# Kernel tuning notes

Measured on AMD Instinct MI355X. Metric: run time of the kernel, lower is better.

The kernel has to match this reference:

```python
import jax, jax.numpy as jnp
import numpy as np

H = 256
EPS = 1e-5
RBF_GAMMA = 10.0
RBF_CENTERS = jnp.asarray(np.arange(0.0, np.pi, 0.1), dtype=jnp.float32)  # 32 centers


def layer_norm(x, g, b):
    m = x.mean(-1, keepdims=True)
    v = ((x - m) ** 2).mean(-1, keepdims=True)
    return (x - m) * jax.lax.rsqrt(v + EPS) * g + b


def gin(src, dst, n_nodes, node_feat, edge_feat, w1, b1, w2, b2):
    # message = h_src + h_edge ; sum-aggregate at dst ; 2-layer MLP
    msg = node_feat[src] + edge_feat                                  # [E, H]
    agg = jax.ops.segment_sum(msg, dst, num_segments=n_nodes)        # [N, H]
    return jax.nn.relu(agg @ w1 + b1) @ w2 + b2


def graph_normal(gid, n_graphs, x):
    # divide each node feature by sqrt(#nodes in its graph)
    cnt = jax.ops.segment_sum(jnp.ones((x.shape[0],), x.dtype), gid, num_segments=n_graphs)
    return x * jax.lax.rsqrt(jnp.maximum(cnt, 1.0))[gid][:, None]


def geognn_block(src, dst, gid, n_graphs, node_hidden, edge_feat, w1, b1, w2, b2, ln_g, ln_b):
    out = gin(src, dst, node_hidden.shape[0], node_hidden, edge_feat, w1, b1, w2, b2)
    out = layer_norm(out, ln_g, ln_b)
    out = graph_normal(gid, n_graphs, out)
    # activation=False, dropout is identity in eval mode
    return out + node_hidden


def setup_inputs() -> dict:
    key = jax.random.key(0)
    ks = jax.random.split(key, 24)
    N, E, A, G = 65536, 131072, 262144, 2048
    nC = RBF_CENTERS.shape[0]
    s = 1.0 / np.sqrt(H)
    inp = {
        "node_hidden": jax.random.normal(ks[0], (N, H), jnp.float32),
        "edge_hidden": jax.random.normal(ks[1], (E, H), jnp.float32),
        "bond_angle": jax.random.uniform(ks[2], (A,), jnp.float32) * np.float32(np.pi),
        "ab_src": jax.random.randint(ks[3], (N * 2,), 0, N).astype(jnp.int64)[:E],
        "ab_dst": jax.random.randint(ks[4], (E,), 0, N).astype(jnp.int64),
        "ba_src": jax.random.randint(ks[5], (A,), 0, E).astype(jnp.int64),
        "ba_dst": jax.random.randint(ks[6], (A,), 0, E).astype(jnp.int64),
        "node_gid": jnp.sort(jax.random.randint(ks[7], (N,), 0, G)).astype(jnp.int64),
        "bond_gid": jnp.sort(jax.random.randint(ks[8], (E,), 0, G)).astype(jnp.int64),
        "num_graphs": G,
        # bond-angle RBF linear
        "rbf_w": jax.random.normal(ks[9], (nC, H), jnp.float32) / np.sqrt(nC),
        "rbf_b": jnp.zeros((H,), jnp.float32),
        # bond_angle_gnn (GIN MLP + LayerNorm)
        "ba_w1": jax.random.normal(ks[10], (H, 2 * H), jnp.float32) * s,
        "ba_b1": jnp.zeros((2 * H,), jnp.float32),
        "ba_w2": jax.random.normal(ks[11], (2 * H, H), jnp.float32) * s,
        "ba_b2": jnp.zeros((H,), jnp.float32),
        "ba_ln_g": jnp.ones((H,), jnp.float32),
        "ba_ln_b": jnp.zeros((H,), jnp.float32),
        # atom_bond_gnn
        "ab_w1": jax.random.normal(ks[12], (H, 2 * H), jnp.float32) * s,
        "ab_b1": jnp.zeros((2 * H,), jnp.float32),
        "ab_w2": jax.random.normal(ks[13], (2 * H, H), jnp.float32) * s,
        "ab_b2": jnp.zeros((H,), jnp.float32),
        "ab_ln_g": jnp.ones((H,), jnp.float32),
        "ab_ln_b": jnp.zeros((H,), jnp.float32),
    }
    return inp


def reference(node_hidden, edge_hidden, bond_angle, ab_src, ab_dst, ba_src, ba_dst,
              node_gid, bond_gid, num_graphs, rbf_w, rbf_b,
              ba_w1, ba_b1, ba_w2, ba_b2, ba_ln_g, ba_ln_b,
              ab_w1, ab_b1, ab_w2, ab_b2, ab_ln_g, ab_ln_b):
    # RBF encode bond angles -> angle edge features [A, H]
    rbf = jnp.exp(-RBF_GAMMA * (bond_angle[:, None] - RBF_CENTERS[None, :]) ** 2)
    angle_hidden = rbf @ rbf_w + rbf_b
    # bond-angle GNN updates bond features (nodes of bond_angle graph)
    edge_out = geognn_block(ba_src, ba_dst, bond_gid, num_graphs,
                            edge_hidden, angle_hidden,
                            ba_w1, ba_b1, ba_w2, ba_b2, ba_ln_g, ba_ln_b)
    # atom-bond GNN updates atom features using updated bond features as edge feats
    node_out = geognn_block(ab_src, ab_dst, node_gid, num_graphs,
                            node_hidden, edge_out,
                            ab_w1, ab_b1, ab_w2, ab_b2, ab_ln_g, ab_ln_b)
    # average pooling over atoms per graph
    cnt = jax.ops.segment_sum(jnp.ones((node_out.shape[0],), node_out.dtype), node_gid,
                              num_segments=num_graphs)
    graph_repr = jax.ops.segment_sum(node_out, node_gid, num_segments=num_graphs) / jnp.maximum(cnt, 1.0)[:, None]
    return node_out, edge_out, graph_repr
```

## Files before the change

kernel.cpp:

```cpp
#include <hip/hip_runtime.h>

#define HDIM 256
#define LNEPS 1e-5f

typedef float f32x4 __attribute__((ext_vector_type(4)));
typedef short bf16x8 __attribute__((ext_vector_type(8)));

static __device__ __forceinline__ unsigned short f2b(float f) {
  union { float f; unsigned u; } v; v.f = f;
  return (unsigned short)((v.u + 0x7fffu + ((v.u >> 16) & 1u)) >> 16);
}
static __device__ __forceinline__ unsigned pk2(float lo, float hi) {
  return (unsigned)f2b(lo) | ((unsigned)f2b(hi) << 16);
}

__global__ void pack_all_kernel(const float* __restrict__ w1a, const float* __restrict__ w2a,
                                const float* __restrict__ w1b, const float* __restrict__ w2b,
                                unsigned short* __restrict__ o1a, unsigned short* __restrict__ o2a,
                                unsigned short* __restrict__ o1b, unsigned short* __restrict__ o2b) {
  int sel = blockIdx.x >> 9;
  int o = (blockIdx.x & 511) * 256 + threadIdx.x;
  if (sel == 0 || sel == 2) {
    const float* in = (sel == 0) ? w1a : w1b;
    unsigned short* out = (sel == 0) ? o1a : o1b;
    int ke = o & 7, n1l = (o >> 3) & 127, lg = (o >> 10) & 3, sl = o >> 12;
    int h = sl >> 3, kk = sl & 7;
    int k = kk * 32 + lg * 8 + ke, n1 = h * 128 + n1l;
    out[o] = f2b(in[k * 512 + n1]);
  } else {
    const float* in = (sel == 1) ? w2a : w2b;
    unsigned short* out = (sel == 1) ? o2a : o2b;
    int ke = o & 7, n2l = (o >> 3) & 127, lg = (o >> 10) & 3, sl = o >> 12;
    int h = sl >> 3, r = sl & 7, h2 = r >> 2, kk2 = r & 3;
    int k2 = h * 128 + kk2 * 32 + lg * 8 + ke, n2 = h2 * 128 + n2l;
    out[o] = f2b(in[k2 * 256 + n2]);
  }
}

__global__ void prep_kernel(const int* __restrict__ node_gid, const int* __restrict__ bond_gid,
                            const int* __restrict__ ab_dst, const int* __restrict__ ba_dst,
                            int* cnt_node, int* cnt_bond, int* deg_n, int* deg_e,
                            int N, int E, int A) {
  int i = blockIdx.x * 256 + threadIdx.x;
  if (i < N) atomicAdd(&cnt_node[node_gid[i]], 1);
  if (i < E) {
    atomicAdd(&cnt_bond[bond_gid[i]], 1);
    atomicAdd(&deg_n[ab_dst[i]], 1);
  }
  if (i < A) atomicAdd(&deg_e[ba_dst[i]], 1);
}

__global__ void scan1_both_kernel(const int* __restrict__ degE, const int* __restrict__ degN,
                                  int* __restrict__ offE, int* __restrict__ offN,
                                  int* __restrict__ bsum, int E, int N, int nbE) {
  int b = blockIdx.x;
  const int* deg; int* excl; int* bs; int n; int bb;
  if (b < nbE) { deg = degE; excl = offE; bs = bsum; n = E; bb = b; }
  else { deg = degN; excl = offN; bs = bsum + 512; n = N; bb = b - nbE; }
  int t = threadIdx.x;
  int i = bb * 256 + t;
  int v = (i < n) ? deg[i] : 0;
  int lane = t & 63, w = t >> 6;
  int s = v;
#pragma unroll
  for (int d = 1; d < 64; d <<= 1) {
    int u = __shfl_up(s, d);
    if (lane >= d) s += u;
  }
  __shared__ int wsum[4];
  if (lane == 63) wsum[w] = s;
  __syncthreads();
  int base = 0;
  for (int ww = 0; ww < w; ++ww) base += wsum[ww];
  if (i < n) excl[i] = base + s - v;
  if (t == 255) bs[bb] = base + s;
}

__global__ void scan2_both_kernel(int* __restrict__ bsum, int nbE, int nbN) {
  int* bs = bsum + blockIdx.x * 512;
  int nb = (blockIdx.x == 0) ? nbE : nbN;
  int t = threadIdx.x;
  int v = (t < nb) ? bs[t] : 0;
  int lane = t & 63, w = t >> 6;
  int s = v;
#pragma unroll
  for (int d = 1; d < 64; d <<= 1) {
    int u = __shfl_up(s, d);
    if (lane >= d) s += u;
  }
  __shared__ int wsum[16];
  if (lane == 63) wsum[w] = s;
  __syncthreads();
  int base = 0;
  for (int ww = 0; ww < w; ++ww) base += wsum[ww];
  if (t < nb) bs[t] = base + s - v;
}

__global__ void scan3f_kernel(int* __restrict__ offE, int* __restrict__ offN,
                              const int* __restrict__ bsum,
                              const int* __restrict__ cnt_node, const int* __restrict__ cnt_bond,
                              float* fac_node, float* fac_bond, float* recip_node,
                              int E, int N, int G, int nbE, int nbN) {
  int b = blockIdx.x;
  if (b < nbE) {
    int i = b * 256 + threadIdx.x;
    if (i < E) offE[i] += bsum[b];
  } else if (b < nbE + nbN) {
    int bb = b - nbE;
    int i = bb * 256 + threadIdx.x;
    if (i < N) offN[i] += bsum[512 + bb];
  } else {
    int g = (b - nbE - nbN) * 256 + threadIdx.x;
    if (g < G) {
      float cn = fmaxf((float)cnt_node[g], 1.f);
      float cb = fmaxf((float)cnt_bond[g], 1.f);
      fac_node[g] = rsqrtf(cn);
      fac_bond[g] = rsqrtf(cb);
      recip_node[g] = 1.f / cn;
    }
  }
}

__global__ void fill_both_kernel(const int* __restrict__ ba_dst, const int* __restrict__ ab_dst,
                                 const int* __restrict__ offE, const int* __restrict__ offN,
                                 int* __restrict__ curE, int* __restrict__ curN,
                                 int* __restrict__ csrE, int* __restrict__ csrN,
                                 int A, int E, int nbA) {
  int b = blockIdx.x;
  if (b < nbA) {
    int i = b * 256 + threadIdx.x;
    if (i < A) {
      int d = ba_dst[i];
      int p = atomicAdd(&curE[d], 1);
      csrE[offE[d] + p] = i;
    }
  } else {
    int i = (b - nbA) * 256 + threadIdx.x;
    if (i < E) {
      int d = ab_dst[i];
      int p = atomicAdd(&curN[d], 1);
      csrN[offN[d] + p] = i;
    }
  }
}

__global__ __launch_bounds__(256) void angle_gather_kernel(
    const float* __restrict__ bond_angle, const int* __restrict__ ba_src,
    const float* __restrict__ edge_hidden,
    const int* __restrict__ off, const int* __restrict__ deg, const int* __restrict__ csr,
    const float* __restrict__ rbf_w, const float* __restrict__ rbf_b,
    float* __restrict__ agg_e, int E) {
  __shared__ float rbfw_s[32 * 256];
  int t = threadIdx.x;
  int w = t >> 6, lane = t & 63;
#pragma unroll
  for (int i = 0; i < 8; ++i)
    *(f32x4*)&rbfw_s[(t + i * 256) * 4] = *(const f32x4*)&rbf_w[(t + i * 256) * 4];
  __syncthreads();
  int c4 = lane * 4;
  f32x4 bv = *(const f32x4*)&rbf_b[c4];
  float cc = 0.1f * (float)(lane & 31);
  for (int rr = 0; rr < 2; ++rr) {
    int d = blockIdx.x * 8 + w * 2 + rr;
    if (d >= E) break;
    int start = off[d], cnt = deg[d];
    f32x4 acc = (f32x4)0.f;
    float rbfs = 0.f;
    for (int base = 0; base < cnt; base += 64) {
      int n = cnt - base; if (n > 64) n = 64;
      float av = 0.f;
      int s = 0;
      if (lane < n) {
        int a = csr[start + base + lane];
        av = bond_angle[a];
        s = ba_src[a];
      }
#pragma unroll 4
      for (int i = 0; i < n; ++i) {
        float avi = __shfl(av, i);
        int si = __shfl(s, i);
        if (lane < 32) {
          float dd = avi - cc;
          rbfs += __expf(-10.f * dd * dd);
        }
        acc += *(const f32x4*)&edge_hidden[(size_t)si * HDIM + c4];
      }
    }
#pragma unroll 8
    for (int k = 0; k < 32; ++k) {
      float rv = __shfl(rbfs, k);
      f32x4 wv = *(const f32x4*)&rbfw_s[k * 256 + c4];
      acc[0] += rv * wv[0]; acc[1] += rv * wv[1];
      acc[2] += rv * wv[2]; acc[3] += rv * wv[3];
    }
    float fc = (float)cnt;
    acc[0] += fc * bv[0]; acc[1] += fc * bv[1];
    acc[2] += fc * bv[2]; acc[3] += fc * bv[3];
    *(f32x4*)&agg_e[(size_t)d * HDIM + c4] = acc;
  }
}

__global__ __launch_bounds__(256) void node_gather_kernel(
    const float* __restrict__ node_hidden, const float* __restrict__ edge_out,
    const int* __restrict__ ab_src,
    const int* __restrict__ off, const int* __restrict__ deg, const int* __restrict__ csr,
    float* __restrict__ agg_n, int N) {
  int w = threadIdx.x >> 6, lane = threadIdx.x & 63;
  int d = blockIdx.x * 4 + w;
  if (d >= N) return;
  int c4 = lane * 4;
  int start = off[d], cnt = deg[d];
  f32x4 acc = (f32x4)0.f;
  for (int base = 0; base < cnt; base += 64) {
    int n = cnt - base; if (n > 64) n = 64;
    int e = 0, s = 0;
    if (lane < n) {
      e = csr[start + base + lane];
      s = ab_src[e];
    }
#pragma unroll 4
    for (int i = 0; i < n; ++i) {
      int ei = __shfl(e, i);
      int si = __shfl(s, i);
      f32x4 a = *(const f32x4*)&edge_out[(size_t)ei * HDIM + c4];
      f32x4 b = *(const f32x4*)&node_hidden[(size_t)si * HDIM + c4];
      acc += a;
      acc += b;
    }
  }
  *(f32x4*)&agg_n[(size_t)d * HDIM + c4] = acc;
}

template <int POOL>
__global__ __launch_bounds__(256, 4) void mlp_kernel(
    const float* agg_in, float* out_rows,
    const float* __restrict__ residual, const int* __restrict__ gid,
    const float* __restrict__ gfactor, const float* __restrict__ grecip,
    const unsigned short* __restrict__ w1p, const float* __restrict__ b1,
    const unsigned short* __restrict__ w2p, const float* __restrict__ b2,
    const float* __restrict__ ln_g, const float* __restrict__ ln_b,
    float* pool_out, int M) {
  __shared__ __align__(16) char smem[40960];
  char* Xb = smem;
  char* Hb = smem + 16384;
  char* Wb = smem + 24576;
  char* OutsB = smem;
  float* psA = (float*)(smem + 32768);
  float* psB = (float*)(smem + 33280);
  float* fstat = (float*)(smem + 33792);
  float* gfs = (float*)(smem + 34048);
  float* grs = (float*)(smem + 34176);
  int* gid_s = (int*)(smem + 34304);

  int t = threadIdx.x;
  int row0 = blockIdx.x * 32;
  int w = t >> 6, lane = t & 63;
  int l15 = lane & 15, lg = lane >> 4;

  auto slab_ptr = [&](int ss) -> const uint4* {
    int hh = ss >> 4, r = ss & 15;
    const unsigned short* p = (r < 8) ? (w1p + (size_t)(hh * 8 + r) * 4096)
                                      : (w2p + (size_t)(hh * 8 + (r - 8)) * 4096);
    return (const uint4*)p;
  };

  uint4 rA0, rA1, rB0, rB1;

  {
    const uint4* g0 = slab_ptr(0);
    uint4 s0a = g0[t], s0b = g0[t + 256];
    const uint4* g1 = slab_ptr(1);
    rA0 = g1[t]; rA1 = g1[t + 256];
    int row = t >> 3;
    int c0 = (t & 7) * 32;
    int gr = row0 + row; if (gr >= M) gr = M - 1;
    const float* src = agg_in + (size_t)gr * HDIM + c0;
#pragma unroll
    for (int i = 0; i < 4; ++i) {
      f32x4 a = *(const f32x4*)(src + i * 8);
      f32x4 b = *(const f32x4*)(src + i * 8 + 4);
      int byte = (row * 512 + (c0 + i * 8) * 2) ^ ((row & 7) << 4);
      *(uint4*)(Xb + byte) =
          make_uint4(pk2(a[0], a[1]), pk2(a[2], a[3]), pk2(b[0], b[1]), pk2(b[2], b[3]));
    }
    *(uint4*)(Wb + t * 16) = s0a;
    *(uint4*)(Wb + (t + 256) * 16) = s0b;
  }
  __syncthreads();

  f32x4 acc2[2][4];
#pragma unroll
  for (int mt = 0; mt < 2; ++mt)
#pragma unroll
    for (int nf = 0; nf < 4; ++nf) acc2[mt][nf] = (f32x4)0.f;

  int s = 0;
  for (int h = 0; h < 4; ++h) {
    f32x4 acc1[2][2];
#pragma unroll
    for (int tt = 0; tt < 2; ++tt)
#pragma unroll
      for (int mt = 0; mt < 2; ++mt) acc1[tt][mt] = (f32x4)0.f;

    for (int kk = 0; kk < 8; ++kk) {
      if (s + 2 < 64) { const uint4* g = slab_ptr(s + 2); rB0 = g[t]; rB1 = g[t + 256]; }
      const char* buf = Wb + (s & 1) * 8192;
      bf16x8 xfr[2], afr[2];
#pragma unroll
      for (int mt = 0; mt < 2; ++mt) {
        int m = mt * 16 + l15;
        int byte = (m * 512 + kk * 64 + lg * 16) ^ ((m & 7) << 4);
        xfr[mt] = *(const bf16x8*)(Xb + byte);
      }
#pragma unroll
      for (int tt = 0; tt < 2; ++tt)
        afr[tt] = *(const bf16x8*)(buf + lg * 2048 + (w * 32 + tt * 16 + l15) * 16);
#pragma unroll
      for (int tt = 0; tt < 2; ++tt)
#pragma unroll
        for (int mt = 0; mt < 2; ++mt)
          acc1[tt][mt] = __builtin_amdgcn_mfma_f32_16x16x32_bf16(afr[tt], xfr[mt], acc1[tt][mt], 0, 0, 0);

      if (kk == 7) {
#pragma unroll
        for (int tt = 0; tt < 2; ++tt) {
          f32x4 b1v = *(const f32x4*)&b1[h * 128 + w * 32 + tt * 16 + lg * 4];
#pragma unroll
          for (int mt = 0; mt < 2; ++mt) {
            f32x4 v = acc1[tt][mt] + b1v;
            v[0] = fmaxf(v[0], 0.f); v[1] = fmaxf(v[1], 0.f);
            v[2] = fmaxf(v[2], 0.f); v[3] = fmaxf(v[3], 0.f);
            int m = mt * 16 + l15;
            int n1l = w * 32 + tt * 16 + lg * 4;
            int byte = (m * 256 + n1l * 2) ^ ((m & 7) << 4);
            *(uint2*)(Hb + byte) = make_uint2(pk2(v[0], v[1]), pk2(v[2], v[3]));
          }
        }
      }
      if (s + 1 < 64) {
        char* nb = Wb + ((s + 1) & 1) * 8192;
        *(uint4*)(nb + t * 16) = rA0;
        *(uint4*)(nb + (t + 256) * 16) = rA1;
      }
      __syncthreads();
      rA0 = rB0; rA1 = rB1;
      ++s;
    }

#pragma unroll
    for (int h2 = 0; h2 < 2; ++h2) {
#pragma unroll
      for (int kk2 = 0; kk2 < 4; ++kk2) {
        if (s + 2 < 64) { const uint4* g = slab_ptr(s + 2); rB0 = g[t]; rB1 = g[t + 256]; }
        const char* buf = Wb + (s & 1) * 8192;
        bf16x8 hfr[2], wfr[2];
#pragma unroll
        for (int mt = 0; mt < 2; ++mt) {
          int m = mt * 16 + l15;
          int byte = (m * 256 + kk2 * 64 + lg * 16) ^ ((m & 7) << 4);
          hfr[mt] = *(const bf16x8*)(Hb + byte);
        }
#pragma unroll
        for (int nf = 0; nf < 2; ++nf)
          wfr[nf] = *(const bf16x8*)(buf + lg * 2048 + (w * 32 + nf * 16 + l15) * 16);
#pragma unroll
        for (int mt = 0; mt < 2; ++mt)
#pragma unroll
          for (int nf = 0; nf < 2; ++nf)
            acc2[mt][h2 * 2 + nf] =
                __builtin_amdgcn_mfma_f32_16x16x32_bf16(hfr[mt], wfr[nf], acc2[mt][h2 * 2 + nf], 0, 0, 0);
        if (s + 1 < 64) {
          char* nb = Wb + ((s + 1) & 1) * 8192;
          *(uint4*)(nb + t * 16) = rA0;
          *(uint4*)(nb + (t + 256) * 16) = rA1;
        }
        __syncthreads();
        rA0 = rB0; rA1 = rB1;
        ++s;
      }
    }
  }

  {
    float rs[2][4], rss[2][4];
#pragma unroll
    for (int mt = 0; mt < 2; ++mt)
#pragma unroll
      for (int jr = 0; jr < 4; ++jr) { rs[mt][jr] = 0.f; rss[mt][jr] = 0.f; }
#pragma unroll
    for (int nfi = 0; nfi < 4; ++nfi) {
      int col = (nfi >> 1) * 128 + w * 32 + (nfi & 1) * 16 + l15;
      float b2v = b2[col];
#pragma unroll
      for (int mt = 0; mt < 2; ++mt)
#pragma unroll
        for (int jr = 0; jr < 4; ++jr) {
          float v = acc2[mt][nfi][jr] + b2v;
          int row = mt * 16 + lg * 4 + jr;
          *(float*)(OutsB + (((row * 256 + col) * 4) ^ ((row & 7) << 4))) = v;
          rs[mt][jr] += v;
          rss[mt][jr] += v * v;
        }
    }
#pragma unroll
    for (int mt = 0; mt < 2; ++mt)
#pragma unroll
      for (int jr = 0; jr < 4; ++jr) {
        float sv = rs[mt][jr], ssv = rss[mt][jr];
        sv += __shfl_xor(sv, 1); ssv += __shfl_xor(ssv, 1);
        sv += __shfl_xor(sv, 2); ssv += __shfl_xor(ssv, 2);
        sv += __shfl_xor(sv, 4); ssv += __shfl_xor(ssv, 4);
        sv += __shfl_xor(sv, 8); ssv += __shfl_xor(ssv, 8);
        if (l15 == 0) {
          int r = mt * 16 + lg * 4 + jr;
          psA[r * 4 + w] = sv;
          psB[r * 4 + w] = ssv;
        }
      }
    if (t < 32) {
      int r = row0 + t;
      int g = (r < M) ? gid[r] : 0;
      gid_s[t] = g;
      gfs[t] = gfactor[g];
      if (POOL) grs[t] = grecip[g];
    }
  }
  __syncthreads();
  if (t < 32) {
    float sv = psA[t * 4] + psA[t * 4 + 1] + psA[t * 4 + 2] + psA[t * 4 + 3];
    float ssv = psB[t * 4] + psB[t * 4 + 1] + psB[t * 4 + 2] + psB[t * 4 + 3];
    float mean = sv * (1.f / 256.f);
    float var = ssv * (1.f / 256.f) - mean * mean;
    fstat[t * 2] = mean;
    fstat[t * 2 + 1] = rsqrtf(var + LNEPS);
  }
  __syncthreads();

  {
    float g_t = ln_g[t], bb_t = ln_b[t];
    float psum = 0.f;
    float currecip = 0.f;
    int curg = -1;
#pragma unroll 4
    for (int p = 0; p < 32; ++p) {
      int gr = row0 + p;
      if (gr < M) {
        float v = *(const float*)(OutsB + (((p * 256 + t) * 4) ^ ((p & 7) << 4)));
        v = (v - fstat[p * 2]) * fstat[p * 2 + 1] * g_t + bb_t;
        v *= gfs[p];
        v += residual[(size_t)gr * HDIM + t];
        out_rows[(size_t)gr * HDIM + t] = v;
        if (POOL) {
          int g = gid_s[p];
          if (g != curg) {
            if (curg >= 0) atomicAdd(&pool_out[(size_t)curg * HDIM + t], psum * currecip);
            psum = 0.f;
            curg = g;
            currecip = grs[p];
          }
          psum += v;
        }
      }
    }
    if (POOL && curg >= 0) atomicAdd(&pool_out[(size_t)curg * HDIM + t], psum * currecip);
  }
}

extern "C" void kernel_launch(void* const* d_in, const int* in_sizes, int n_in,
                              void* d_out, int out_size, void* d_ws, size_t ws_size,
                              hipStream_t stream) {
  const float* node_hidden = (const float*)d_in[0];
  const float* edge_hidden = (const float*)d_in[1];
  const float* bond_angle = (const float*)d_in[2];
  const int* ab_src = (const int*)d_in[3];
  const int* ab_dst = (const int*)d_in[4];
  const int* ba_src = (const int*)d_in[5];
  const int* ba_dst = (const int*)d_in[6];
  const int* node_gid = (const int*)d_in[7];
  const int* bond_gid = (const int*)d_in[8];
  const float* rbf_w = (const float*)d_in[10];
  const float* rbf_b = (const float*)d_in[11];
  const float* ba_w1 = (const float*)d_in[12];
  const float* ba_b1 = (const float*)d_in[13];
  const float* ba_w2 = (const float*)d_in[14];
  const float* ba_b2 = (const float*)d_in[15];
  const float* ba_ln_g = (const float*)d_in[16];
  const float* ba_ln_b = (const float*)d_in[17];
  const float* ab_w1 = (const float*)d_in[18];
  const float* ab_b1 = (const float*)d_in[19];
  const float* ab_w2 = (const float*)d_in[20];
  const float* ab_b2 = (const float*)d_in[21];
  const float* ab_ln_g = (const float*)d_in[22];
  const float* ab_ln_b = (const float*)d_in[23];

  int N = in_sizes[0] / HDIM;
  int E = in_sizes[1] / HDIM;
  int A = in_sizes[2];
  int G = out_size / HDIM - N - E;

  float* out_node = (float*)d_out;
  float* out_edge = out_node + (size_t)N * HDIM;
  float* out_graph = out_edge + (size_t)E * HDIM;

  char* ws = (char*)d_ws;
  int* cnt_node = (int*)ws;
  int* cnt_bond = cnt_node + G;
  int* deg_e = cnt_bond + G;
  int* cur_e = deg_e + E;
  int* deg_n = cur_e + E;
  int* cur_n = deg_n + N;
  size_t zero_bytes = (size_t)(2 * G + 2 * E + 2 * N) * 4;
  float* fac_node = (float*)(cur_n + N);
  float* fac_bond = fac_node + G;
  float* recip_node = fac_bond + G;
  int* off_e = (int*)(recip_node + G);
  int* csr_e = off_e + E;
  int* off_n = csr_e + A;
  int* csr_n = off_n + N;
  int* bsum = csr_n + E;
  size_t off = ((size_t)((char*)(bsum + 1024) - ws) + 255) & ~(size_t)255;
  unsigned short* w1p_ba = (unsigned short*)(ws + off); off += (size_t)512 * 256 * 2;
  unsigned short* w2p_ba = (unsigned short*)(ws + off); off += (size_t)256 * 512 * 2;
  unsigned short* w1p_ab = (unsigned short*)(ws + off); off += (size_t)512 * 256 * 2;
  unsigned short* w2p_ab = (unsigned short*)(ws + off); off += (size_t)256 * 512 * 2;

  hipMemsetAsync(d_ws, 0, zero_bytes, stream);
  hipMemsetAsync(out_graph, 0, (size_t)G * HDIM * 4, stream);

  pack_all_kernel<<<2048, 256, 0, stream>>>(ba_w1, ba_w2, ab_w1, ab_w2,
                                            w1p_ba, w2p_ba, w1p_ab, w2p_ab);

  prep_kernel<<<(A + 255) / 256, 256, 0, stream>>>(node_gid, bond_gid, ab_dst, ba_dst,
                                                   cnt_node, cnt_bond, deg_n, deg_e, N, E, A);

  int nbE = (E + 255) / 256;
  int nbN = (N + 255) / 256;
  int nbA = (A + 255) / 256;
  int nbG = (G + 255) / 256;
  scan1_both_kernel<<<nbE + nbN, 256, 0, stream>>>(deg_e, deg_n, off_e, off_n, bsum, E, N, nbE);
  scan2_both_kernel<<<2, 1024, 0, stream>>>(bsum, nbE, nbN);
  scan3f_kernel<<<nbE + nbN + nbG, 256, 0, stream>>>(off_e, off_n, bsum, cnt_node, cnt_bond,
                                                     fac_node, fac_bond, recip_node,
                                                     E, N, G, nbE, nbN);
  fill_both_kernel<<<nbA + nbE, 256, 0, stream>>>(ba_dst, ab_dst, off_e, off_n,
                                                  cur_e, cur_n, csr_e, csr_n, A, E, nbA);

  angle_gather_kernel<<<(E + 7) / 8, 256, 0, stream>>>(bond_angle, ba_src, edge_hidden,
                                                       off_e, deg_e, csr_e, rbf_w, rbf_b,
                                                       out_edge, E);
  mlp_kernel<0><<<(E + 31) / 32, 256, 0, stream>>>(out_edge, out_edge, edge_hidden, bond_gid,
                                                   fac_bond, nullptr, w1p_ba, ba_b1, w2p_ba,
                                                   ba_b2, ba_ln_g, ba_ln_b, nullptr, E);

  node_gather_kernel<<<(N + 3) / 4, 256, 0, stream>>>(node_hidden, out_edge, ab_src,
                                                      off_n, deg_n, csr_n, out_node, N);
  mlp_kernel<1><<<(N + 31) / 32, 256, 0, stream>>>(out_node, out_node, node_hidden, node_gid,
                                                   fac_node, recip_node, w1p_ab, ab_b1, w2p_ab,
                                                   ab_b2, ab_ln_g, ab_ln_b, out_graph, N);
}
```

Before: 597.5 us.

## Double MLP row tile to 64 rows with 512-thread blocks and 2x4 warp grid

The fused MLP+LayerNorm kernel now processes 64 rows per block with 8 waves arranged as 2 row groups by 4 column groups, instead of 32 rows with 4 waves. Each streamed bf16 weight slab is loaded cooperatively with one uint4 per thread and reused across twice as many rows. This halves the weight traffic from global memory and the per-row cost of the slab barriers. In exchange, LDS grows to about 68 KB per block and blocks are larger, which reduces the number of resident blocks per CU and makes the grid coarser.

```diff
diff --git a/kernel.cpp b/kernel.cpp
--- a/kernel.cpp
+++ b/kernel.cpp
@@ -232,7 +232,7 @@
 }
 
 template <int POOL>
-__global__ __launch_bounds__(256, 4) void mlp_kernel(
+__global__ __launch_bounds__(512, 4) void mlp_kernel(
     const float* agg_in, float* out_rows,
     const float* __restrict__ residual, const int* __restrict__ gid,
     const float* __restrict__ gfactor, const float* __restrict__ grecip,
@@ -240,21 +240,22 @@
     const unsigned short* __restrict__ w2p, const float* __restrict__ b2,
     const float* __restrict__ ln_g, const float* __restrict__ ln_b,
     float* pool_out, int M) {
-  __shared__ __align__(16) char smem[40960];
+  __shared__ __align__(16) char smem[69632];
   char* Xb = smem;
-  char* Hb = smem + 16384;
-  char* Wb = smem + 24576;
+  char* Hb = smem + 32768;
+  char* Wb = smem + 49152;
   char* OutsB = smem;
-  float* psA = (float*)(smem + 32768);
-  float* psB = (float*)(smem + 33280);
-  float* fstat = (float*)(smem + 33792);
-  float* gfs = (float*)(smem + 34048);
-  float* grs = (float*)(smem + 34176);
-  int* gid_s = (int*)(smem + 34304);
+  float* psA = (float*)(smem + 65536);
+  float* psB = (float*)(smem + 66560);
+  float* fstat = (float*)(smem + 67584);
+  float* gfs = (float*)(smem + 68096);
+  float* grs = (float*)(smem + 68352);
+  int* gid_s = (int*)(smem + 68608);
 
   int t = threadIdx.x;
-  int row0 = blockIdx.x * 32;
-  int w = t >> 6, lane = t & 63;
+  int row0 = blockIdx.x * 64;
+  int w8 = t >> 6, lane = t & 63;
+  int wr = w8 >> 2, wc = w8 & 3;
   int l15 = lane & 15, lg = lane >> 4;
 
   auto slab_ptr = [&](int ss) -> const uint4* {
@@ -264,13 +265,12 @@
     return (const uint4*)p;
   };
 
-  uint4 rA0, rA1, rB0, rB1;
+  uint4 rA0, rB0;
 
   {
     const uint4* g0 = slab_ptr(0);
-    uint4 s0a = g0[t], s0b = g0[t + 256];
-    const uint4* g1 = slab_ptr(1);
-    rA0 = g1[t]; rA1 = g1[t + 256];
+    uint4 s0a = g0[t];
+    rA0 = slab_ptr(1)[t];
     int row = t >> 3;
     int c0 = (t & 7) * 32;
     int gr = row0 + row; if (gr >= M) gr = M - 1;
@@ -284,7 +284,6 @@
           make_uint4(pk2(a[0], a[1]), pk2(a[2], a[3]), pk2(b[0], b[1]), pk2(b[2], b[3]));
     }
     *(uint4*)(Wb + t * 16) = s0a;
-    *(uint4*)(Wb + (t + 256) * 16) = s0b;
   }
   __syncthreads();
 
@@ -303,18 +302,18 @@
       for (int mt = 0; mt < 2; ++mt) acc1[tt][mt] = (f32x4)0.f;
 
     for (int kk = 0; kk < 8; ++kk) {
-      if (s + 2 < 64) { const uint4* g = slab_ptr(s + 2); rB0 = g[t]; rB1 = g[t + 256]; }
+      if (s + 2 < 64) rB0 = slab_ptr(s + 2)[t];
       const char* buf = Wb + (s & 1) * 8192;
       bf16x8 xfr[2], afr[2];
 #pragma unroll
       for (int mt = 0; mt < 2; ++mt) {
-        int m = mt * 16 + l15;
+        int m = wr * 32 + mt * 16 + l15;
         int byte = (m * 512 + kk * 64 + lg * 16) ^ ((m & 7) << 4);
         xfr[mt] = *(const bf16x8*)(Xb + byte);
       }
 #pragma unroll
       for (int tt = 0; tt < 2; ++tt)
-        afr[tt] = *(const bf16x8*)(buf + lg * 2048 + (w * 32 + tt * 16 + l15) * 16);
+        afr[tt] = *(const bf16x8*)(buf + lg * 2048 + (wc * 32 + tt * 16 + l15) * 16);
 #pragma unroll
       for (int tt = 0; tt < 2; ++tt)
 #pragma unroll
@@ -324,14 +323,14 @@
       if (kk == 7) {
 #pragma unroll
         for (int tt = 0; tt < 2; ++tt) {
-          f32x4 b1v = *(const f32x4*)&b1[h * 128 + w * 32 + tt * 16 + lg * 4];
+          f32x4 b1v = *(const f32x4*)&b1[h * 128 + wc * 32 + tt * 16 + lg * 4];
 #pragma unroll
           for (int mt = 0; mt < 2; ++mt) {
             f32x4 v = acc1[tt][mt] + b1v;
             v[0] = fmaxf(v[0], 0.f); v[1] = fmaxf(v[1], 0.f);
             v[2] = fmaxf(v[2], 0.f); v[3] = fmaxf(v[3], 0.f);
-            int m = mt * 16 + l15;
-            int n1l = w * 32 + tt * 16 + lg * 4;
+            int m = wr * 32 + mt * 16 + l15;
+            int n1l = wc * 32 + tt * 16 + lg * 4;
             int byte = (m * 256 + n1l * 2) ^ ((m & 7) << 4);
             *(uint2*)(Hb + byte) = make_uint2(pk2(v[0], v[1]), pk2(v[2], v[3]));
           }
@@ -340,10 +339,9 @@
       if (s + 1 < 64) {
         char* nb = Wb + ((s + 1) & 1) * 8192;
         *(uint4*)(nb + t * 16) = rA0;
-        *(uint4*)(nb + (t + 256) * 16) = rA1;
       }
       __syncthreads();
-      rA0 = rB0; rA1 = rB1;
+      rA0 = rB0;
       ++s;
     }
 
@@ -351,18 +349,18 @@
     for (int h2 = 0; h2 < 2; ++h2) {
 #pragma unroll
       for (int kk2 = 0; kk2 < 4; ++kk2) {
-        if (s + 2 < 64) { const uint4* g = slab_ptr(s + 2); rB0 = g[t]; rB1 = g[t + 256]; }
+        if (s + 2 < 64) rB0 = slab_ptr(s + 2)[t];
         const char* buf = Wb + (s & 1) * 8192;
         bf16x8 hfr[2], wfr[2];
 #pragma unroll
         for (int mt = 0; mt < 2; ++mt) {
-          int m = mt * 16 + l15;
+          int m = wr * 32 + mt * 16 + l15;
           int byte = (m * 256 + kk2 * 64 + lg * 16) ^ ((m & 7) << 4);
           hfr[mt] = *(const bf16x8*)(Hb + byte);
         }
 #pragma unroll
         for (int nf = 0; nf < 2; ++nf)
-          wfr[nf] = *(const bf16x8*)(buf + lg * 2048 + (w * 32 + nf * 16 + l15) * 16);
+          wfr[nf] = *(const bf16x8*)(buf + lg * 2048 + (wc * 32 + nf * 16 + l15) * 16);
 #pragma unroll
         for (int mt = 0; mt < 2; ++mt)
 #pragma unroll
@@ -372,10 +370,9 @@
         if (s + 1 < 64) {
           char* nb = Wb + ((s + 1) & 1) * 8192;
           *(uint4*)(nb + t * 16) = rA0;
-          *(uint4*)(nb + (t + 256) * 16) = rA1;
         }
         __syncthreads();
-        rA0 = rB0; rA1 = rB1;
+        rA0 = rB0;
         ++s;
       }
     }
@@ -389,14 +386,14 @@
       for (int jr = 0; jr < 4; ++jr) { rs[mt][jr] = 0.f; rss[mt][jr] = 0.f; }
 #pragma unroll
     for (int nfi = 0; nfi < 4; ++nfi) {
-      int col = (nfi >> 1) * 128 + w * 32 + (nfi & 1) * 16 + l15;
+      int col = (nfi >> 1) * 128 + wc * 32 + (nfi & 1) * 16 + l15;
       float b2v = b2[col];
 #pragma unroll
       for (int mt = 0; mt < 2; ++mt)
 #pragma unroll
         for (int jr = 0; jr < 4; ++jr) {
           float v = acc2[mt][nfi][jr] + b2v;
-          int row = mt * 16 + lg * 4 + jr;
+          int row = wr * 32 + mt * 16 + lg * 4 + jr;
           *(float*)(OutsB + (((row * 256 + col) * 4) ^ ((row & 7) << 4))) = v;
           rs[mt][jr] += v;
           rss[mt][jr] += v * v;
@@ -412,12 +409,12 @@
         sv += __shfl_xor(sv, 4); ssv += __shfl_xor(ssv, 4);
         sv += __shfl_xor(sv, 8); ssv += __shfl_xor(ssv, 8);
         if (l15 == 0) {
-          int r = mt * 16 + lg * 4 + jr;
-          psA[r * 4 + w] = sv;
-          psB[r * 4 + w] = ssv;
-        }
-      }
-    if (t < 32) {
+          int r = wr * 32 + mt * 16 + lg * 4 + jr;
+          psA[r * 4 + wc] = sv;
+          psB[r * 4 + wc] = ssv;
+        }
+      }
+    if (t < 64) {
       int r = row0 + t;
       int g = (r < M) ? gid[r] : 0;
       gid_s[t] = g;
@@ -426,7 +423,7 @@
     }
   }
   __syncthreads();
-  if (t < 32) {
+  if (t < 64) {
     float sv = psA[t * 4] + psA[t * 4 + 1] + psA[t * 4 + 2] + psA[t * 4 + 3];
     float ssv = psB[t * 4] + psB[t * 4 + 1] + psB[t * 4 + 2] + psB[t * 4 + 3];
     float mean = sv * (1.f / 256.f);
@@ -437,23 +434,25 @@
   __syncthreads();
 
   {
-    float g_t = ln_g[t], bb_t = ln_b[t];
+    int colf = t & 255;
+    int p0 = (t >> 8) * 32;
+    float g_t = ln_g[colf], bb_t = ln_b[colf];
     float psum = 0.f;
     float currecip = 0.f;
     int curg = -1;
 #pragma unroll 4
-    for (int p = 0; p < 32; ++p) {
+    for (int p = p0; p < p0 + 32; ++p) {
       int gr = row0 + p;
       if (gr < M) {
-        float v = *(const float*)(OutsB + (((p * 256 + t) * 4) ^ ((p & 7) << 4)));
+        float v = *(const float*)(OutsB + (((p * 256 + colf) * 4) ^ ((p & 7) << 4)));
         v = (v - fstat[p * 2]) * fstat[p * 2 + 1] * g_t + bb_t;
         v *= gfs[p];
-        v += residual[(size_t)gr * HDIM + t];
-        out_rows[(size_t)gr * HDIM + t] = v;
+        v += residual[(size_t)gr * HDIM + colf];
+        out_rows[(size_t)gr * HDIM + colf] = v;
         if (POOL) {
           int g = gid_s[p];
           if (g != curg) {
-            if (curg >= 0) atomicAdd(&pool_out[(size_t)curg * HDIM + t], psum * currecip);
+            if (curg >= 0) atomicAdd(&pool_out[(size_t)curg * HDIM + colf], psum * currecip);
             psum = 0.f;
             curg = g;
             currecip = grs[p];
@@ -462,7 +461,7 @@
         }
       }
     }
-    if (POOL && curg >= 0) atomicAdd(&pool_out[(size_t)curg * HDIM + t], psum * currecip);
+    if (POOL && curg >= 0) atomicAdd(&pool_out[(size_t)curg * HDIM + colf], psum * currecip);
   }
 }
 
@@ -548,13 +547,13 @@
   angle_gather_kernel<<<(E + 7) / 8, 256, 0, stream>>>(bond_angle, ba_src, edge_hidden,
                                                        off_e, deg_e, csr_e, rbf_w, rbf_b,
                                                        out_edge, E);
-  mlp_kernel<0><<<(E + 31) / 32, 256, 0, stream>>>(out_edge, out_edge, edge_hidden, bond_gid,
+  mlp_kernel<0><<<(E + 63) / 64, 512, 0, stream>>>(out_edge, out_edge, edge_hidden, bond_gid,
                                                    fac_bond, nullptr, w1p_ba, ba_b1, w2p_ba,
                                                    ba_b2, ba_ln_g, ba_ln_b, nullptr, E);
 
   node_gather_kernel<<<(N + 3) / 4, 256, 0, stream>>>(node_hidden, out_edge, ab_src,
                                                       off_n, deg_n, csr_n, out_node, N);
-  mlp_kernel<1><<<(N + 31) / 32, 256, 0, stream>>>(out_node, out_node, node_hidden, node_gid,
+  mlp_kernel<1><<<(N + 63) / 64, 512, 0, stream>>>(out_node, out_node, node_hidden, node_gid,
                                                    fac_node, recip_node, w1p_ab, ab_b1, w2p_ab,
                                                    ab_b2, ab_ln_g, ab_ln_b, out_graph, N);
 }
```

Result: no change. 586.5 us (-1.8%).
